# Kernel tuning notes

Measured on AMD Instinct MI355X. Metric: run time of the kernel, lower is better.

Reference implementation:

```python
import jax, jax.numpy as jnp
import numpy as np

N = 100000
E = 1600000
F_IN = 32
HID = 16
C_OUT = 10
K = 4


def setup_inputs() -> dict:
    key = jax.random.key(0)
    k1, k2, k3, k4, k5, k6, k7 = jax.random.split(key, 7)
    x = jax.random.normal(k1, (N, F_IN), dtype=jnp.float32)
    edge_index = jax.random.randint(k2, (2, E), 0, N, dtype=jnp.int64)
    # ChebConv weights: one [in, out] matrix per Chebyshev order k
    W1 = jax.random.normal(k3, (K, F_IN, HID), dtype=jnp.float32) / np.sqrt(F_IN)
    b1 = jax.random.normal(k4, (HID,), dtype=jnp.float32) * 0.01
    W2 = jax.random.normal(k5, (K, HID, C_OUT), dtype=jnp.float32) / np.sqrt(HID)
    b2 = jax.random.normal(k6, (C_OUT,), dtype=jnp.float32) * 0.01
    return {"x": x, "edge_index": edge_index, "W1": W1, "b1": b1, "W2": W2, "b2": b2}


def _cheb_conv(h, src, dst, norm, W, b, num_nodes):
    # Tx_0 = h; Tx_1 = L_hat h; Tx_k = 2 L_hat Tx_{k-1} - Tx_{k-2}
    def prop(v):  # v: [N, F] -> L_hat v via sparse gather/scatter
        return jax.ops.segment_sum(norm[:, None] * v[src], dst, num_segments=num_nodes)

    Tx0 = h
    out = Tx0 @ W[0]
    Tx1 = prop(h)
    out = out + Tx1 @ W[1]
    for k in range(2, W.shape[0]):
        Tx2 = 2.0 * prop(Tx1) - Tx0
        out = out + Tx2 @ W[k]
        Tx0, Tx1 = Tx1, Tx2
    return out + b


def reference(x, edge_index, W1, b1, W2, b2):
    src, dst = edge_index[0], edge_index[1]
    num_nodes = x.shape[0]
    # symmetric normalization with lambda_max = 2: L_hat = -D^{-1/2} A D^{-1/2}
    deg = jax.ops.segment_sum(jnp.ones((src.shape[0],), dtype=x.dtype), dst, num_segments=num_nodes)
    dis = jnp.where(deg > 0, jax.lax.rsqrt(jnp.maximum(deg, 1.0)), 0.0)
    norm = -dis[src] * dis[dst]
    h = _cheb_conv(x, src, dst, norm, W1, b1, num_nodes)
    h = jax.nn.relu(h)
    # dropout is identity in eval mode
    h = _cheb_conv(h, src, dst, norm, W2, b2, num_nodes)
    return jax.nn.log_softmax(h, axis=1)
```

## Files before the change

kernel.cpp:

```cpp
#include <hip/hip_runtime.h>
#include <hip/hip_bf16.h>
#include <math.h>


#define BLK 256
#define BLKP 512
#define NBUCK_MAX 256
#define CHUNK 8192
#define CAPB 16384
#define PLACE_CAP 10240

__device__ inline unsigned short f32_to_bf16_rne(float f) {
    unsigned int u = __float_as_uint(f);
    unsigned int rounding = 0x7FFFu + ((u >> 16) & 1u);
    return (unsigned short)((u + rounding) >> 16);
}
__device__ inline unsigned int pack_bf16x2(float a, float b) {
    return (unsigned int)f32_to_bf16_rne(a) | ((unsigned int)f32_to_bf16_rne(b) << 16);
}
__device__ inline void unpack8(const uint4 u, float* f) {
    const unsigned int* p = &u.x;
#pragma unroll
    for (int j = 0; j < 4; j++) {
        unsigned int w = p[j];
        f[2 * j]     = __uint_as_float(w << 16);
        f[2 * j + 1] = __uint_as_float(w & 0xFFFF0000u);
    }
}
__device__ inline void add8(const uint4 u, float* acc) {
    const unsigned int* p = &u.x;
#pragma unroll
    for (int j = 0; j < 4; j++) {
        unsigned int w = p[j];
        acc[2 * j]     += __uint_as_float(w << 16);
        acc[2 * j + 1] += __uint_as_float(w & 0xFFFF0000u);
    }
}
__device__ inline uint4 pack8(const float* r) {
    uint4 o;
    o.x = pack_bf16x2(r[0], r[1]);
    o.y = pack_bf16x2(r[2], r[3]);
    o.z = pack_bf16x2(r[4], r[5]);
    o.w = pack_bf16x2(r[6], r[7]);
    return o;
}

__device__ inline void fma8_w8(const uint4 u, float s, const float* __restrict__ W,
                               float* acc) {
    const unsigned int* p = &u.x;
#pragma unroll
    for (int q = 0; q < 4; q++) {
        float fa = __uint_as_float(p[q] << 16) * s;
        float fb = __uint_as_float(p[q] & 0xFFFF0000u) * s;
        const float* Wa = W + (2 * q) * 16;
        const float* Wb = W + (2 * q + 1) * 16;
#pragma unroll
        for (int j = 0; j < 8; j++) acc[j] += fa * Wa[j] + fb * Wb[j];
    }
}
__device__ inline void fma8_w10(const uint4 u, float s, const float* __restrict__ W,
                                float* acc) {
    const unsigned int* p = &u.x;
#pragma unroll
    for (int q = 0; q < 4; q++) {
        float fa = __uint_as_float(p[q] << 16) * s;
        float fb = __uint_as_float(p[q] & 0xFFFF0000u) * s;
        const float* Wa = W + (2 * q) * 10;
        const float* Wb = W + (2 * q + 1) * 10;
#pragma unroll
        for (int j = 0; j < 10; j++) acc[j] += fa * Wa[j] + fb * Wb[j];
    }
}

__global__ __launch_bounds__(BLK)
void binned_scatter_kernel(const int* __restrict__ src, const int* __restrict__ dst,
                           int* __restrict__ bfill, int* __restrict__ tmp,
                           int E, int nbuck) {
    __shared__ int cnt[NBUCK_MAX];
    __shared__ int lofs[NBUCK_MAX + 1];
    __shared__ int pos[NBUCK_MAX];
    __shared__ int gbase[NBUCK_MAX];
    __shared__ int stage[CHUNK];
    __shared__ unsigned char bkt[CHUNK];

    int tid = threadIdx.x;
    int e0 = blockIdx.x * CHUNK;
    int nE = min(CHUNK, E - e0);

    for (int b = tid; b < nbuck; b += BLK) { cnt[b] = 0; pos[b] = 0; }
    __syncthreads();

    for (int i = tid; i < nE; i += BLK) {
        int d = dst[e0 + i];
        atomicAdd(&cnt[d >> 9], 1);
    }
    __syncthreads();

    {
        int v = (tid < nbuck) ? cnt[tid] : 0;
        lofs[tid] = v;
        __syncthreads();
        for (int off = 1; off < BLK; off <<= 1) {
            int t = (tid >= off) ? lofs[tid - off] : 0;
            __syncthreads();
            lofs[tid] += t;
            __syncthreads();
        }
        int incl = lofs[tid];
        __syncthreads();
        lofs[tid] = incl - v;
        if (tid == 0) lofs[nbuck] = nE;
        if (tid < nbuck && v > 0)
            gbase[tid] = tid * CAPB + atomicAdd(&bfill[tid], v);
    }
    __syncthreads();

    for (int i = tid; i < nE; i += BLK) {
        int s = src[e0 + i];
        int d = dst[e0 + i];
        int b = d >> 9;
        int slot = lofs[b] + atomicAdd(&pos[b], 1);
        stage[slot] = (s << 9) | (d & 511);
        bkt[slot] = (unsigned char)b;
    }
    __syncthreads();

    for (int i = tid; i < nE; i += BLK) {
        int b = bkt[i];
        tmp[gbase[b] + (i - lofs[b])] = stage[i];
    }
}

__global__ __launch_bounds__(BLKP)
void bucket_place_kernel(const int* __restrict__ bfill, const int* __restrict__ tmp,
                         int* __restrict__ psrc, int* __restrict__ rowbeg,
                         int* __restrict__ rowend, float* __restrict__ dis,
                         float* __restrict__ d2, float* __restrict__ inv, int N) {
    __shared__ int cnt[512];
    __shared__ int ofs[512];
    __shared__ int fill[512];
    __shared__ int stage[PLACE_CAP];

    int b = blockIdx.x;
    int tid = threadIdx.x;
    int n0 = b << 9;
    int nn = min(512, N - n0);
    int S = b * CAPB;
    int tot = bfill[b];

    cnt[tid] = 0;
    fill[tid] = 0;
    __syncthreads();

    for (int i = tid; i < tot; i += BLKP) atomicAdd(&cnt[tmp[S + i] & 511], 1);
    __syncthreads();

    int v = cnt[tid];
    ofs[tid] = v;
    __syncthreads();
    for (int off = 1; off < 512; off <<= 1) {
        int t = (tid >= off) ? ofs[tid - off] : 0;
        __syncthreads();
        ofs[tid] += t;
        __syncthreads();
    }
    int excl = ofs[tid] - v;
    __syncthreads();
    ofs[tid] = excl;
    if (tid < nn) {
        rowbeg[n0 + tid] = S + excl;
        rowend[n0 + tid] = S + excl + v;
        float fv = (float)v;
        dis[n0 + tid] = (v > 0) ? rsqrtf(fv) : 0.0f;
        d2[n0 + tid]  = (v > 0) ? 1.0f / fv : 0.0f;
        inv[n0 + tid] = (v > 0) ? sqrtf(fv) : 0.0f;
    }
    __syncthreads();

    if (tot <= PLACE_CAP) {
        for (int i = tid; i < tot; i += BLKP) {
            int rec = tmp[S + i];
            int nl = rec & 511;
            int slot = ofs[nl] + atomicAdd(&fill[nl], 1);
            stage[slot] = rec >> 9;
        }
        __syncthreads();
        for (int i = tid; i < tot; i += BLKP) psrc[S + i] = stage[i];
    } else {
        for (int i = tid; i < tot; i += BLKP) {
            int rec = tmp[S + i];
            int nl = rec & 511;
            int slot = S + ofs[nl] + atomicAdd(&fill[nl], 1);
            psrc[slot] = rec >> 9;
        }
    }
}

__global__ __launch_bounds__(BLK)
void cvt_u0_kernel(const float* __restrict__ x, const float* __restrict__ dis,
                   uint4* __restrict__ u0, int N) {
    int t = blockIdx.x * blockDim.x + threadIdx.x;
    if (t >= N * 4) return;
    int n = t >> 2;
    int c = t & 3;
    float dn = dis[n];
    const float4* in4 = reinterpret_cast<const float4*>(x + (size_t)n * 32 + c * 8);
    float4 a = in4[0], b = in4[1];
    float r[8] = {dn * a.x, dn * a.y, dn * a.z, dn * a.w,
                  dn * b.x, dn * b.y, dn * b.z, dn * b.w};
    u0[(size_t)n * 4 + c] = pack8(r);
}

template <int C, bool HAVE_PREV>
__global__ __launch_bounds__(BLK)
void prop_u_kernel(const int* __restrict__ rowbeg, const int* __restrict__ rowend,
                   const int* __restrict__ psrc, const float* __restrict__ d2,
                   const uint4* __restrict__ vb, const uint4* __restrict__ prevb,
                   uint4* __restrict__ outb, float scale, int N) {
    int t = blockIdx.x * blockDim.x + threadIdx.x;
    int n = t / C;
    int c = t % C;
    if (n >= N) return;
    int beg = rowbeg[n];
    int end = rowend[n];
    float acc[8];
#pragma unroll
    for (int j = 0; j < 8; j++) acc[j] = 0.f;
    int i = beg;
    for (; i + 3 < end; i += 4) {
        int s0 = psrc[i], s1 = psrc[i + 1], s2 = psrc[i + 2], s3 = psrc[i + 3];
        uint4 a0 = vb[(size_t)s0 * C + c];
        uint4 a1 = vb[(size_t)s1 * C + c];
        uint4 a2 = vb[(size_t)s2 * C + c];
        uint4 a3 = vb[(size_t)s3 * C + c];
        add8(a0, acc);
        add8(a1, acc);
        add8(a2, acc);
        add8(a3, acc);
    }
    for (; i < end; i++) {
        uint4 a0 = vb[(size_t)psrc[i] * C + c];
        add8(a0, acc);
    }
    float f = -scale * d2[n];
    float r[8];
    if (HAVE_PREV) {
        float p[8];
        unpack8(prevb[(size_t)n * C + c], p);
#pragma unroll
        for (int j = 0; j < 8; j++) r[j] = f * acc[j] - p[j];
    } else {
#pragma unroll
        for (int j = 0; j < 8; j++) r[j] = f * acc[j];
    }
    outb[(size_t)n * C + c] = pack8(r);
}

__global__ __launch_bounds__(BLK)
void combine1_kernel(const float* __restrict__ x, const uint4* __restrict__ u1,
                     const uint4* __restrict__ u2, const uint4* __restrict__ u3,
                     const float* __restrict__ inv, const float* __restrict__ dis,
                     const float* __restrict__ W1, const float* __restrict__ b1,
                     uint4* __restrict__ hb, uint4* __restrict__ uh, int N) {
    __shared__ float sW[4 * 32 * 16];
    __shared__ float sb[16];
    for (int i = threadIdx.x; i < 4 * 32 * 16; i += blockDim.x) sW[i] = W1[i];
    if (threadIdx.x < 16) sb[threadIdx.x] = b1[threadIdx.x];
    __syncthreads();
    int t = blockIdx.x * blockDim.x + threadIdx.x;
    int n = t >> 1;
    int h = t & 1;
    if (n >= N) return;
    const float* sWh = sW + h * 8;
    float acc[8];
#pragma unroll
    for (int j = 0; j < 8; j++) acc[j] = sb[h * 8 + j];
    {
        const float4* in4 = reinterpret_cast<const float4*>(x + (size_t)n * 32);
#pragma unroll
        for (int q = 0; q < 8; q++) {
            float4 a = in4[q];
            const float* Wq = sWh + q * 4 * 16;
#pragma unroll
            for (int j = 0; j < 8; j++)
                acc[j] += a.x * Wq[j] + a.y * Wq[16 + j] + a.z * Wq[32 + j] + a.w * Wq[48 + j];
        }
    }
    float iv = inv[n];
#pragma unroll
    for (int c = 0; c < 4; c++) fma8_w8(u1[(size_t)n * 4 + c], iv, sWh + 512 + c * 128, acc);
#pragma unroll
    for (int c = 0; c < 4; c++) fma8_w8(u2[(size_t)n * 4 + c], iv, sWh + 1024 + c * 128, acc);
#pragma unroll
    for (int c = 0; c < 4; c++) fma8_w8(u3[(size_t)n * 4 + c], iv, sWh + 1536 + c * 128, acc);
    if (iv == 0.0f) {
        const float4* in4 = reinterpret_cast<const float4*>(x + (size_t)n * 32);
#pragma unroll
        for (int q = 0; q < 8; q++) {
            float4 a = in4[q];
            const float* Wq = sWh + 1024 + q * 4 * 16;
#pragma unroll
            for (int j = 0; j < 8; j++)
                acc[j] -= a.x * Wq[j] + a.y * Wq[16 + j] + a.z * Wq[32 + j] + a.w * Wq[48 + j];
        }
    }
    float dn = dis[n];
    float r[8], u[8];
#pragma unroll
    for (int j = 0; j < 8; j++) {
        r[j] = fmaxf(acc[j], 0.0f);
        u[j] = dn * r[j];
    }
    hb[(size_t)n * 2 + h] = pack8(r);
    uh[(size_t)n * 2 + h] = pack8(u);
}

__global__ __launch_bounds__(BLK)
void combine2_kernel(const uint4* __restrict__ hb, const uint4* __restrict__ us1,
                     const uint4* __restrict__ us2, const uint4* __restrict__ us3,
                     const float* __restrict__ inv,
                     const float* __restrict__ W2, const float* __restrict__ b2,
                     float* __restrict__ out, int N) {
    __shared__ float sW[4 * 16 * 10];
    __shared__ float sb[10];
    for (int i = threadIdx.x; i < 4 * 16 * 10; i += blockDim.x) sW[i] = W2[i];
    if (threadIdx.x < 10) sb[threadIdx.x] = b2[threadIdx.x];
    __syncthreads();
    int n = blockIdx.x * blockDim.x + threadIdx.x;
    if (n >= N) return;
    float acc[10];
#pragma unroll
    for (int c = 0; c < 10; c++) acc[c] = sb[c];
    float iv = inv[n];
#pragma unroll
    for (int c = 0; c < 2; c++) fma8_w10(hb[(size_t)n * 2 + c],  1.0f, sW + c * 80, acc);
#pragma unroll
    for (int c = 0; c < 2; c++) fma8_w10(us1[(size_t)n * 2 + c], iv, sW + 160 + c * 80, acc);
#pragma unroll
    for (int c = 0; c < 2; c++) fma8_w10(us2[(size_t)n * 2 + c], iv, sW + 320 + c * 80, acc);
#pragma unroll
    for (int c = 0; c < 2; c++) fma8_w10(us3[(size_t)n * 2 + c], iv, sW + 480 + c * 80, acc);
    if (iv == 0.0f) {
#pragma unroll
        for (int c = 0; c < 2; c++) fma8_w10(hb[(size_t)n * 2 + c], -1.0f, sW + 320 + c * 80, acc);
    }
    float m = acc[0];
#pragma unroll
    for (int c = 1; c < 10; c++) m = fmaxf(m, acc[c]);
    float sum = 0.0f;
#pragma unroll
    for (int c = 0; c < 10; c++) sum += expf(acc[c] - m);
    float lse = m + logf(sum);
    float* o = out + (size_t)n * 10;
#pragma unroll
    for (int c = 0; c < 10; c++) o[c] = acc[c] - lse;
}

extern "C" void kernel_launch(void* const* d_in, const int* in_sizes, int n_in,
                              void* d_out, int out_size, void* d_ws, size_t ws_size,
                              hipStream_t stream) {
    const float* x  = (const float*)d_in[0];
    const int*   ei = (const int*)d_in[1];
    const float* W1 = (const float*)d_in[2];
    const float* b1 = (const float*)d_in[3];
    const float* W2 = (const float*)d_in[4];
    const float* b2 = (const float*)d_in[5];
    float* out = (float*)d_out;

    const int N = in_sizes[0] / 32;
    const int E = in_sizes[1] / 2;
    const int* src = ei;
    const int* dst = ei + E;

    const int nbuck = (N + 511) / 512;

    char* w = (char*)d_ws;
    int*   bfill  = (int*)w;              w += NBUCK_MAX * 4;
    int*   rowbeg = (int*)w;              w += (size_t)(N + 4) * 4;
    int*   rowend = (int*)w;              w += (size_t)(N + 4) * 4;
    float* dis    = (float*)w;            w += (size_t)N * 4;
    float* d2     = (float*)w;            w += (size_t)N * 4;
    float* inv    = (float*)w;            w += (size_t)N * 4;
    int*   tmp    = (int*)w;              w += (size_t)NBUCK_MAX * CAPB * 4;
    int*   psrc   = (int*)w;              w += (size_t)NBUCK_MAX * CAPB * 4;
    uint4* u0     = (uint4*)w;            w += (size_t)64 * N;
    uint4* u1     = (uint4*)w;            w += (size_t)64 * N;
    uint4* u2     = (uint4*)w;            w += (size_t)64 * N;
    uint4* u3     = (uint4*)w;            w += (size_t)64 * N;
    uint4* hb     = (uint4*)w;            w += (size_t)32 * N;
    uint4* uh     = (uint4*)w;            w += (size_t)32 * N;
    uint4* us1    = (uint4*)w;            w += (size_t)32 * N;
    uint4* us2    = (uint4*)w;            w += (size_t)32 * N;
    uint4* us3    = (uint4*)w;            w += (size_t)32 * N;

    int gN   = (N + BLK - 1) / BLK;
    int gN2  = (N * 2 + BLK - 1) / BLK;
    int gU32 = (N * 4 + BLK - 1) / BLK;
    int gU16 = (N * 2 + BLK - 1) / BLK;
    int gCH  = (E + CHUNK - 1) / CHUNK;

    hipMemsetAsync(bfill, 0, NBUCK_MAX * sizeof(int), stream);
    binned_scatter_kernel<<<gCH, BLK, 0, stream>>>(src, dst, bfill, tmp, E, nbuck);
    bucket_place_kernel<<<nbuck, BLKP, 0, stream>>>(bfill, tmp, psrc, rowbeg, rowend,
                                                    dis, d2, inv, N);

    cvt_u0_kernel<<<gU32, BLK, 0, stream>>>(x, dis, u0, N);
    prop_u_kernel<4, false><<<gU32, BLK, 0, stream>>>(rowbeg, rowend, psrc, d2, u0, nullptr, u1, 1.0f, N);
    prop_u_kernel<4, true ><<<gU32, BLK, 0, stream>>>(rowbeg, rowend, psrc, d2, u1, u0,      u2, 2.0f, N);
    prop_u_kernel<4, true ><<<gU32, BLK, 0, stream>>>(rowbeg, rowend, psrc, d2, u2, u1,      u3, 2.0f, N);
    combine1_kernel<<<gN2, BLK, 0, stream>>>(x, u1, u2, u3, inv, dis, W1, b1, hb, uh, N);

    prop_u_kernel<2, false><<<gU16, BLK, 0, stream>>>(rowbeg, rowend, psrc, d2, uh,  nullptr, us1, 1.0f, N);
    prop_u_kernel<2, true ><<<gU16, BLK, 0, stream>>>(rowbeg, rowend, psrc, d2, us1, uh,      us2, 2.0f, N);
    prop_u_kernel<2, true ><<<gU16, BLK, 0, stream>>>(rowbeg, rowend, psrc, d2, us2, us1,     us3, 2.0f, N);
    combine2_kernel<<<gN, BLK, 0, stream>>>(hb, us1, us2, us3, inv, W2, b2, out, N);
}
```

Baseline: 292.5 us.

## Pad CSR rows to multiples of four with zero sentinel node and vector index loads

Each destination row in the CSR edge list is padded to a multiple of four entries, and the padding points at an extra sentinel node N whose feature rows are zeroed in every propagation buffer. This lets the propagation loop drop its scalar remainder loop and fetch four source indices with one 16-byte load. Nontemporal loads and stores are also applied to the scatter staging buffer, the edge index reads and the previous-term reads. In exchange it adds padded-edge gathers of the zero row, extra buffer space, and a small zeroing step inside the conversion kernel.

```diff
diff --git a/kernel.cpp b/kernel.cpp
--- a/kernel.cpp
+++ b/kernel.cpp
@@ -10,6 +10,9 @@
 #define CAPB 16384
 #define PLACE_CAP 10240
 
+typedef int vec4i __attribute__((ext_vector_type(4)));
+typedef unsigned int vec4u __attribute__((ext_vector_type(4)));
+
 __device__ inline unsigned short f32_to_bf16_rne(float f) {
     unsigned int u = __float_as_uint(f);
     unsigned int rounding = 0x7FFFu + ((u >> 16) & 1u);
@@ -18,11 +21,10 @@
 __device__ inline unsigned int pack_bf16x2(float a, float b) {
     return (unsigned int)f32_to_bf16_rne(a) | ((unsigned int)f32_to_bf16_rne(b) << 16);
 }
-__device__ inline void unpack8(const uint4 u, float* f) {
-    const unsigned int* p = &u.x;
+__device__ inline void unpack8v(const vec4u u, float* f) {
 #pragma unroll
     for (int j = 0; j < 4; j++) {
-        unsigned int w = p[j];
+        unsigned int w = u[j];
         f[2 * j]     = __uint_as_float(w << 16);
         f[2 * j + 1] = __uint_as_float(w & 0xFFFF0000u);
     }
@@ -127,7 +129,7 @@
 
     for (int i = tid; i < nE; i += BLK) {
         int b = bkt[i];
-        tmp[gbase[b] + (i - lofs[b])] = stage[i];
+        __builtin_nontemporal_store(stage[i], &tmp[gbase[b] + (i - lofs[b])]);
     }
 }
 
@@ -140,6 +142,7 @@
     __shared__ int ofs[512];
     __shared__ int fill[512];
     __shared__ int stage[PLACE_CAP];
+    __shared__ int totpad_s;
 
     int b = blockIdx.x;
     int tid = threadIdx.x;
@@ -156,7 +159,8 @@
     __syncthreads();
 
     int v = cnt[tid];
-    ofs[tid] = v;
+    int vp = (v + 3) & ~3;
+    ofs[tid] = vp;
     __syncthreads();
     for (int off = 1; off < 512; off <<= 1) {
         int t = (tid >= off) ? ofs[tid - off] : 0;
@@ -164,51 +168,78 @@
         ofs[tid] += t;
         __syncthreads();
     }
-    int excl = ofs[tid] - v;
+    if (tid == 511) totpad_s = ofs[511];
+    int excl = ofs[tid] - vp;
     __syncthreads();
     ofs[tid] = excl;
     if (tid < nn) {
         rowbeg[n0 + tid] = S + excl;
-        rowend[n0 + tid] = S + excl + v;
+        rowend[n0 + tid] = S + excl + vp;
         float fv = (float)v;
         dis[n0 + tid] = (v > 0) ? rsqrtf(fv) : 0.0f;
         d2[n0 + tid]  = (v > 0) ? 1.0f / fv : 0.0f;
         inv[n0 + tid] = (v > 0) ? sqrtf(fv) : 0.0f;
     }
     __syncthreads();
-
-    if (tot <= PLACE_CAP) {
+    int totpad = totpad_s;
+
+    if (totpad <= PLACE_CAP) {
         for (int i = tid; i < tot; i += BLKP) {
-            int rec = tmp[S + i];
+            int rec = __builtin_nontemporal_load(&tmp[S + i]);
             int nl = rec & 511;
             int slot = ofs[nl] + atomicAdd(&fill[nl], 1);
             stage[slot] = rec >> 9;
         }
+        if (tid < nn) {
+            int e = ofs[tid];
+            for (int j = v; j < vp; j++) stage[e + j] = N;
+        }
         __syncthreads();
-        for (int i = tid; i < tot; i += BLKP) psrc[S + i] = stage[i];
+        for (int i = tid; i < totpad; i += BLKP) psrc[S + i] = stage[i];
     } else {
         for (int i = tid; i < tot; i += BLKP) {
-            int rec = tmp[S + i];
+            int rec = __builtin_nontemporal_load(&tmp[S + i]);
             int nl = rec & 511;
             int slot = S + ofs[nl] + atomicAdd(&fill[nl], 1);
             psrc[slot] = rec >> 9;
         }
+        if (tid < nn) {
+            int e = S + ofs[tid];
+            for (int j = v; j < vp; j++) psrc[e + j] = N;
+        }
     }
 }
 
 __global__ __launch_bounds__(BLK)
 void cvt_u0_kernel(const float* __restrict__ x, const float* __restrict__ dis,
-                   uint4* __restrict__ u0, int N) {
+                   uint4* __restrict__ u0, uint4* __restrict__ u1,
+                   uint4* __restrict__ u2, uint4* __restrict__ u3,
+                   uint4* __restrict__ uh, uint4* __restrict__ us1,
+                   uint4* __restrict__ us2, uint4* __restrict__ us3, int N) {
     int t = blockIdx.x * blockDim.x + threadIdx.x;
-    if (t >= N * 4) return;
-    int n = t >> 2;
-    int c = t & 3;
-    float dn = dis[n];
-    const float4* in4 = reinterpret_cast<const float4*>(x + (size_t)n * 32 + c * 8);
-    float4 a = in4[0], b = in4[1];
-    float r[8] = {dn * a.x, dn * a.y, dn * a.z, dn * a.w,
-                  dn * b.x, dn * b.y, dn * b.z, dn * b.w};
-    u0[(size_t)n * 4 + c] = pack8(r);
+    if (t < N * 4) {
+        int n = t >> 2;
+        int c = t & 3;
+        float dn = dis[n];
+        const float4* in4 = reinterpret_cast<const float4*>(x + (size_t)n * 32 + c * 8);
+        float4 a = in4[0], b = in4[1];
+        float r[8] = {dn * a.x, dn * a.y, dn * a.z, dn * a.w,
+                      dn * b.x, dn * b.y, dn * b.z, dn * b.w};
+        u0[(size_t)n * 4 + c] = pack8(r);
+        return;
+    }
+    int ex = t - N * 4;
+    if (ex < 24) {
+        uint4 z = make_uint4(0, 0, 0, 0);
+        if (ex < 16) {
+            uint4* tb[4] = {u0, u1, u2, u3};
+            tb[ex >> 2][(size_t)N * 4 + (ex & 3)] = z;
+        } else {
+            uint4* tb[4] = {uh, us1, us2, us3};
+            int e2 = ex - 16;
+            tb[e2 >> 1][(size_t)N * 2 + (e2 & 1)] = z;
+        }
+    }
 }
 
 template <int C, bool HAVE_PREV>
@@ -226,27 +257,24 @@
     float acc[8];
 #pragma unroll
     for (int j = 0; j < 8; j++) acc[j] = 0.f;
-    int i = beg;
-    for (; i + 3 < end; i += 4) {
-        int s0 = psrc[i], s1 = psrc[i + 1], s2 = psrc[i + 2], s3 = psrc[i + 3];
-        uint4 a0 = vb[(size_t)s0 * C + c];
-        uint4 a1 = vb[(size_t)s1 * C + c];
-        uint4 a2 = vb[(size_t)s2 * C + c];
-        uint4 a3 = vb[(size_t)s3 * C + c];
+    for (int i = beg; i < end; i += 4) {
+        vec4i e = __builtin_nontemporal_load(reinterpret_cast<const vec4i*>(psrc + i));
+        uint4 a0 = vb[(size_t)e.x * C + c];
+        uint4 a1 = vb[(size_t)e.y * C + c];
+        uint4 a2 = vb[(size_t)e.z * C + c];
+        uint4 a3 = vb[(size_t)e.w * C + c];
         add8(a0, acc);
         add8(a1, acc);
         add8(a2, acc);
         add8(a3, acc);
     }
-    for (; i < end; i++) {
-        uint4 a0 = vb[(size_t)psrc[i] * C + c];
-        add8(a0, acc);
-    }
     float f = -scale * d2[n];
     float r[8];
     if (HAVE_PREV) {
+        vec4u pv = __builtin_nontemporal_load(
+            reinterpret_cast<const vec4u*>(prevb + (size_t)n * C + c));
         float p[8];
-        unpack8(prevb[(size_t)n * C + c], p);
+        unpack8v(pv, p);
 #pragma unroll
         for (int j = 0; j < 8; j++) r[j] = f * acc[j] - p[j];
     } else {
@@ -380,23 +408,24 @@
     int*   rowend = (int*)w;              w += (size_t)(N + 4) * 4;
     float* dis    = (float*)w;            w += (size_t)N * 4;
     float* d2     = (float*)w;            w += (size_t)N * 4;
-    float* inv    = (float*)w;            w += (size_t)N * 4;
+    float* inv    = (float*)w;            w += (size_t)(N + 4) * 4;
     int*   tmp    = (int*)w;              w += (size_t)NBUCK_MAX * CAPB * 4;
     int*   psrc   = (int*)w;              w += (size_t)NBUCK_MAX * CAPB * 4;
-    uint4* u0     = (uint4*)w;            w += (size_t)64 * N;
-    uint4* u1     = (uint4*)w;            w += (size_t)64 * N;
-    uint4* u2     = (uint4*)w;            w += (size_t)64 * N;
-    uint4* u3     = (uint4*)w;            w += (size_t)64 * N;
-    uint4* hb     = (uint4*)w;            w += (size_t)32 * N;
-    uint4* uh     = (uint4*)w;            w += (size_t)32 * N;
-    uint4* us1    = (uint4*)w;            w += (size_t)32 * N;
-    uint4* us2    = (uint4*)w;            w += (size_t)32 * N;
-    uint4* us3    = (uint4*)w;            w += (size_t)32 * N;
+    uint4* u0     = (uint4*)w;            w += (size_t)64 * (N + 1);
+    uint4* u1     = (uint4*)w;            w += (size_t)64 * (N + 1);
+    uint4* u2     = (uint4*)w;            w += (size_t)64 * (N + 1);
+    uint4* u3     = (uint4*)w;            w += (size_t)64 * (N + 1);
+    uint4* hb     = (uint4*)w;            w += (size_t)32 * (N + 1);
+    uint4* uh     = (uint4*)w;            w += (size_t)32 * (N + 1);
+    uint4* us1    = (uint4*)w;            w += (size_t)32 * (N + 1);
+    uint4* us2    = (uint4*)w;            w += (size_t)32 * (N + 1);
+    uint4* us3    = (uint4*)w;            w += (size_t)32 * (N + 1);
 
     int gN   = (N + BLK - 1) / BLK;
     int gN2  = (N * 2 + BLK - 1) / BLK;
     int gU32 = (N * 4 + BLK - 1) / BLK;
     int gU16 = (N * 2 + BLK - 1) / BLK;
+    int gCVT = (N * 4 + 24 + BLK - 1) / BLK;
     int gCH  = (E + CHUNK - 1) / CHUNK;
 
     hipMemsetAsync(bfill, 0, NBUCK_MAX * sizeof(int), stream);
@@ -404,7 +433,7 @@
     bucket_place_kernel<<<nbuck, BLKP, 0, stream>>>(bfill, tmp, psrc, rowbeg, rowend,
                                                     dis, d2, inv, N);
 
-    cvt_u0_kernel<<<gU32, BLK, 0, stream>>>(x, dis, u0, N);
+    cvt_u0_kernel<<<gCVT, BLK, 0, stream>>>(x, dis, u0, u1, u2, u3, uh, us1, us2, us3, N);
     prop_u_kernel<4, false><<<gU32, BLK, 0, stream>>>(rowbeg, rowend, psrc, d2, u0, nullptr, u1, 1.0f, N);
     prop_u_kernel<4, true ><<<gU32, BLK, 0, stream>>>(rowbeg, rowend, psrc, d2, u1, u0,      u2, 2.0f, N);
     prop_u_kernel<4, true ><<<gU32, BLK, 0, stream>>>(rowbeg, rowend, psrc, d2, u2, u1,      u3, 2.0f, N);
```

Result: slower. 317.4 us (+8.5%).
